# Performance work log

Hardware: AMD Instinct MI355X
Metric: run time of the kernel (lower is better)

Reference implementation:

```python
import jax, jax.numpy as jnp
import numpy as np

B, S, D, H = 2, 2048, 1024, 16
DH = D // H  # 64, matches Attention's hardcoded d_k=64 scale


def setup_inputs() -> dict:
    key = jax.random.key(0)
    kq, kk, kv, kw, kb = jax.random.split(key, 5)
    return {
        "q": jax.random.normal(kq, (B, S, D), dtype=jnp.float32),
        "k": jax.random.normal(kk, (B, S, D), dtype=jnp.float32),
        "v": jax.random.normal(kv, (B, S, D), dtype=jnp.float32),
        "w_o_w": jax.random.normal(kw, (D, D), dtype=jnp.float32) * 0.02,
        "w_o_b": jax.random.normal(kb, (D,), dtype=jnp.float32) * 0.02,
    }


def _to_heads(x):
    # [B,S,D] -> [B,H,S,DH]
    b, s, d = x.shape
    return x.reshape(b, s, H, DH).transpose(0, 2, 1, 3)


def reference(q, k, v, w_o_w, w_o_b):
    # pre-activation (F.relu) on raw q,k,v
    qh = _to_heads(jax.nn.relu(q))
    kh = _to_heads(jax.nn.relu(k))
    vh = _to_heads(jax.nn.relu(v))
    scale = 1.0 / jnp.sqrt(jnp.asarray(DH, dtype=q.dtype))
    # naive attention: full [B,H,S,S] score matrix, softmax over keys
    scores = jnp.einsum("bhsd,bhtd->bhst", qh, kh) * scale
    probs = jax.nn.softmax(scores, axis=-1)
    attn = jnp.einsum("bhst,bhtd->bhsd", probs, vh)
    # merge heads: [B,H,S,DH] -> [B,S,D]
    out = attn.transpose(0, 2, 1, 3).reshape(B, S, D)
    # output projection (nn.Linear applies x @ W.T + b) then post-activation
    out = out @ w_o_w.T + w_o_b
    return jax.nn.relu(out)
```

## Files before the change

kernel.cpp:

```cpp
#include <hip/hip_runtime.h>
#include <hip/hip_bf16.h>

#define Bc 2
#define Hc 16
#define Sc 2048
#define Dc 1024

typedef __attribute__((ext_vector_type(8))) short s16x8;
typedef __attribute__((ext_vector_type(4))) float f32x4;
typedef __attribute__((ext_vector_type(16))) float f32x16;

#define AS1 __attribute__((address_space(1)))
#define AS3 __attribute__((address_space(3)))

static __device__ __forceinline__ float fexp2(float x) {
#if __has_builtin(__builtin_amdgcn_exp2f)
    return __builtin_amdgcn_exp2f(x);
#else
    float r; asm("v_exp_f32 %0, %1" : "=v"(r) : "v"(x)); return r;
#endif
}

static __device__ __forceinline__ unsigned cvtpk(float lo, float hi) {
    unsigned r; asm("v_cvt_pk_bf16_f32 %0, %1, %2" : "=v"(r) : "v"(lo), "v"(hi));
    return r;
}

static __device__ __forceinline__ void plswap(unsigned &x, unsigned &y) {
#if __has_builtin(__builtin_amdgcn_permlane32_swap)
    typedef __attribute__((ext_vector_type(2))) unsigned int u32x2;
    u32x2 t = __builtin_amdgcn_permlane32_swap(x, y, false, false);
    x = t.x; y = t.y;
#else
    asm volatile("v_permlane32_swap_b32 %0, %1" : "+v"(x), "+v"(y));
#endif
}

static __device__ __forceinline__ unsigned short f2bf(float f) {
    union { float f; unsigned u; } x; x.f = f;
    unsigned r = x.u + 0x7fffu + ((x.u >> 16) & 1u);
    return (unsigned short)(r >> 16);
}

__global__ __launch_bounds__(256) void relu_cvt_heads(const float* __restrict__ src,
                                                      unsigned short* __restrict__ dst,
                                                      float scale) {
    long i = ((long)blockIdx.x * blockDim.x + threadIdx.x) * 4;
    if (i >= (long)Bc * Sc * Dc) return;
    int dh = (int)(i & 63);
    int h  = (int)((i >> 6) & (Hc - 1));
    int s  = (int)((i >> 10) & (Sc - 1));
    int b  = (int)(i >> 21);
    float4 v = *reinterpret_cast<const float4*>(src + i);
    long o = (((long)b * Hc + h) * Sc + s) * 64 + dh;
    ushort4 w;
    w.x = f2bf(fmaxf(v.x, 0.f) * scale);
    w.y = f2bf(fmaxf(v.y, 0.f) * scale);
    w.z = f2bf(fmaxf(v.z, 0.f) * scale);
    w.w = f2bf(fmaxf(v.w, 0.f) * scale);
    *reinterpret_cast<ushort4*>(dst + o) = w;
}

__global__ __launch_bounds__(256) void relu_cvt_vT(const float* __restrict__ v,
                                                   unsigned short* __restrict__ vt) {
    __shared__ unsigned short lds[64][66];
    const int tid = threadIdx.x;
    const int st = blockIdx.x & (Sc / 64 - 1);
    const int bh = blockIdx.x >> 5;
    const int b = bh >> 4, h = bh & 15;
#pragma unroll
    for (int i = 0; i < 4; ++i) {
        int srow = (tid >> 4) + i * 16;
        int scol = (tid & 15) * 4;
        float4 x = *(const float4*)(v + ((long)b * Sc + st * 64 + srow) * Dc + h * 64 + scol);
        lds[srow][scol + 0] = f2bf(fmaxf(x.x, 0.f));
        lds[srow][scol + 1] = f2bf(fmaxf(x.y, 0.f));
        lds[srow][scol + 2] = f2bf(fmaxf(x.z, 0.f));
        lds[srow][scol + 3] = f2bf(fmaxf(x.w, 0.f));
    }
    __syncthreads();
#pragma unroll
    for (int i = 0; i < 2; ++i) {
        int dh = (tid >> 3) + i * 32;
        int sc = (tid & 7) * 8;
        union { unsigned short u[8]; s16x8 v8; } o;
#pragma unroll
        for (int j = 0; j < 8; ++j) o.u[j] = lds[sc + j][dh];
        *(s16x8*)(vt + ((long)bh * 64 + dh) * Sc + st * 64 + sc) = o.v8;
    }
}

__global__ __launch_bounds__(256) void cvt_w(const float* __restrict__ src,
                                             unsigned short* __restrict__ dst) {
    long i = ((long)blockIdx.x * blockDim.x + threadIdx.x) * 4;
    if (i >= (long)Dc * Dc) return;
    float4 v = *reinterpret_cast<const float4*>(src + i);
    ushort4 w;
    w.x = f2bf(v.x); w.y = f2bf(v.y); w.z = f2bf(v.z); w.w = f2bf(v.w);
    *reinterpret_cast<ushort4*>(dst + i) = w;
}

__global__ __launch_bounds__(256, 2) void attn_lds(const unsigned short* __restrict__ qh,
                                                   const unsigned short* __restrict__ kh,
                                                   const unsigned short* __restrict__ vt,
                                                   unsigned short* __restrict__ xout) {
    __shared__ unsigned short Klds[2][64 * 64];
    __shared__ unsigned short Vlds[2][64 * 64];

    const int tid = threadIdx.x;
    const int l = tid & 63, w = tid >> 6;
    const int r32 = l & 31, hl = l >> 5;
    const int job = (blockIdx.x & 7) * 64 + (blockIdx.x >> 3);
    const int qb = job & 15;
    const int bh = job >> 4;

    const unsigned short* Qp = qh + ((long)bh * Sc + qb * 128 + w * 32) * 64;
    const unsigned short* Kp = kh + (long)bh * Sc * 64;
    const unsigned short* Vp = vt + (long)bh * 64 * Sc;

    s16x8 qbf[4];
#pragma unroll
    for (int ds = 0; ds < 4; ++ds)
        qbf[ds] = *(const s16x8*)(Qp + r32 * 64 + ds * 16 + hl * 8);

    f32x16 acc0 = {0,0,0,0,0,0,0,0,0,0,0,0,0,0,0,0};
    f32x16 acc1 = {0,0,0,0,0,0,0,0,0,0,0,0,0,0,0,0};
    float denom = 0.f;

    auto stage = [&](int buf, int kv0) {
#pragma unroll
        for (int j = 0; j < 2; ++j) {
            const int cbase = w * 64 + j * 256;
            const int chunk = cbase + l;
            const int row = chunk >> 3, cc = chunk & 7;
            const int scc = cc ^ (row & 7);
            const unsigned short* ksrc = Kp + (long)(kv0 + row) * 64 + scc * 8;
            const unsigned short* vsrc = Vp + (long)row * Sc + kv0 + scc * 8;
            __builtin_amdgcn_global_load_lds((const AS1 unsigned int*)(const void*)ksrc,
                                             (AS3 unsigned int*)(void*)&Klds[buf][cbase * 8],
                                             16, 0, 0);
            __builtin_amdgcn_global_load_lds((const AS1 unsigned int*)(const void*)vsrc,
                                             (AS3 unsigned int*)(void*)&Vlds[buf][cbase * 8],
                                             16, 0, 0);
        }
    };

    auto compute = [&](int buf) {
        const unsigned short* KB = &Klds[buf][0];
        const unsigned short* VB = &Vlds[buf][0];
        unsigned Bw[4][4];
#pragma unroll
        for (int kt = 0; kt < 2; ++kt) {
            f32x16 st = {0,0,0,0,0,0,0,0,0,0,0,0,0,0,0,0};
#pragma unroll
            for (int ds = 0; ds < 4; ++ds) {
                const int row = kt * 32 + r32;
                const int cc = ((ds * 2 + hl) ^ (row & 7));
                s16x8 ka = *(const s16x8*)(KB + row * 64 + cc * 8);
                st = __builtin_amdgcn_mfma_f32_32x32x16_bf16(ka, qbf[ds], st, 0, 0, 0);
            }
            float p[16];
#pragma unroll
            for (int i = 0; i < 16; ++i) p[i] = fexp2(st[i]);
            denom += (((p[0] + p[1]) + (p[2] + p[3])) + ((p[4] + p[5]) + (p[6] + p[7])))
                   + (((p[8] + p[9]) + (p[10] + p[11])) + ((p[12] + p[13]) + (p[14] + p[15])));
            unsigned a0 = cvtpk(p[0], p[1]),   b0 = cvtpk(p[2], p[3]);
            unsigned c0 = cvtpk(p[4], p[5]),   d0 = cvtpk(p[6], p[7]);
            unsigned a1 = cvtpk(p[8], p[9]),   b1 = cvtpk(p[10], p[11]);
            unsigned c1 = cvtpk(p[12], p[13]), d1 = cvtpk(p[14], p[15]);
            plswap(a0, c0); plswap(b0, d0);
            plswap(a1, c1); plswap(b1, d1);
            Bw[kt * 2 + 0][0] = a0; Bw[kt * 2 + 0][1] = b0;
            Bw[kt * 2 + 0][2] = c0; Bw[kt * 2 + 0][3] = d0;
            Bw[kt * 2 + 1][0] = a1; Bw[kt * 2 + 1][1] = b1;
            Bw[kt * 2 + 1][2] = c1; Bw[kt * 2 + 1][3] = d1;
        }
#pragma unroll
        for (int dt = 0; dt < 2; ++dt) {
#pragma unroll
            for (int s = 0; s < 4; ++s) {
                const int row = dt * 32 + r32;
                const int cc = ((s * 2 + hl) ^ (row & 7));
                s16x8 va = *(const s16x8*)(VB + row * 64 + cc * 8);
                union { unsigned u[4]; s16x8 v8; } bp;
                bp.u[0] = Bw[s][0]; bp.u[1] = Bw[s][1];
                bp.u[2] = Bw[s][2]; bp.u[3] = Bw[s][3];
                if (dt == 0)
                    acc0 = __builtin_amdgcn_mfma_f32_32x32x16_bf16(va, bp.v8, acc0, 0, 0, 0);
                else
                    acc1 = __builtin_amdgcn_mfma_f32_32x32x16_bf16(va, bp.v8, acc1, 0, 0, 0);
            }
        }
    };

    stage(0, 0);
    __syncthreads();
    int cur = 0;
    for (int t = 0; t < Sc / 64 - 1; ++t) {
        stage(cur ^ 1, (t + 1) * 64);
        compute(cur);
        __syncthreads();
        cur ^= 1;
    }
    compute(cur);

    float dn = denom + __shfl_xor(denom, 32);
    const float inv = 1.0f / dn;
    const int b = bh >> 4, h = bh & 15;
    unsigned short* Xrow = xout + ((long)b * Sc + qb * 128 + w * 32 + r32) * Dc + h * 64;
#pragma unroll
    for (int dt = 0; dt < 2; ++dt) {
        const f32x16& A = dt ? acc1 : acc0;
#pragma unroll
        for (int rg = 0; rg < 4; ++rg) {
            unsigned wlo = cvtpk(A[rg * 4 + 0] * inv, A[rg * 4 + 1] * inv);
            unsigned whi = cvtpk(A[rg * 4 + 2] * inv, A[rg * 4 + 3] * inv);
            uint2 wv; wv.x = wlo; wv.y = whi;
            *reinterpret_cast<uint2*>(Xrow + dt * 32 + rg * 8 + hl * 4) = wv;
        }
    }
}

__global__ __launch_bounds__(256, 2) void proj128(const unsigned short* __restrict__ X,
                                                  const unsigned short* __restrict__ Wb,
                                                  const float* __restrict__ bias,
                                                  float* __restrict__ out) {
    __shared__ unsigned short Xlds[2][128 * 64];
    __shared__ unsigned short Wlds[2][64 * 64];

    const int tid = threadIdx.x;
    const int l = tid & 63, w = tid >> 6;
    const int r32 = l & 31, hl = l >> 5;
    const int job = (blockIdx.x & 7) * 64 + (blockIdx.x >> 3);
    const int nb = job & 15;
    const int mb = job >> 4;

    const unsigned short* Xp = X + (long)mb * 128 * Dc;
    const unsigned short* Wp = Wb + (long)nb * 64 * Dc;

    f32x16 acc0 = {0,0,0,0,0,0,0,0,0,0,0,0,0,0,0,0};
    f32x16 acc1 = {0,0,0,0,0,0,0,0,0,0,0,0,0,0,0,0};

    auto stage = [&](int buf, int k0) {
#pragma unroll
        for (int j = 0; j < 4; ++j) {
            const int cbase = w * 256 + j * 64;
            const int chunk = cbase + l;
            const int row = chunk >> 3, cc = chunk & 7;
            const int scc = cc ^ (row & 7);
            const unsigned short* xsrc = Xp + (long)row * Dc + k0 + scc * 8;
            __builtin_amdgcn_global_load_lds((const AS1 unsigned int*)(const void*)xsrc,
                                             (AS3 unsigned int*)(void*)&Xlds[buf][cbase * 8],
                                             16, 0, 0);
        }
#pragma unroll
        for (int j = 0; j < 2; ++j) {
            const int cbase = w * 128 + j * 64;
            const int chunk = cbase + l;
            const int row = chunk >> 3, cc = chunk & 7;
            const int scc = cc ^ (row & 7);
            const unsigned short* wsrc = Wp + (long)row * Dc + k0 + scc * 8;
            __builtin_amdgcn_global_load_lds((const AS1 unsigned int*)(const void*)wsrc,
                                             (AS3 unsigned int*)(void*)&Wlds[buf][cbase * 8],
                                             16, 0, 0);
        }
    };

    auto compute = [&](int buf) {
        const unsigned short* XB = &Xlds[buf][0];
        const unsigned short* WB = &Wlds[buf][0];
#pragma unroll
        for (int ks = 0; ks < 4; ++ks) {
            const int arow = w * 32 + r32;
            const int acc_ = ((ks * 2 + hl) ^ (arow & 7));
            s16x8 af = *(const s16x8*)(XB + arow * 64 + acc_ * 8);
#pragma unroll
            for (int nt = 0; nt < 2; ++nt) {
                const int brow = nt * 32 + r32;
                const int bcc = ((ks * 2 + hl) ^ (brow & 7));
                s16x8 bf = *(const s16x8*)(WB + brow * 64 + bcc * 8);
                if (nt == 0)
                    acc0 = __builtin_amdgcn_mfma_f32_32x32x16_bf16(af, bf, acc0, 0, 0, 0);
                else
                    acc1 = __builtin_amdgcn_mfma_f32_32x32x16_bf16(af, bf, acc1, 0, 0, 0);
            }
        }
    };

    stage(0, 0);
    __syncthreads();
    int cur = 0;
    for (int t = 0; t < Dc / 64 - 1; ++t) {
        stage(cur ^ 1, (t + 1) * 64);
        compute(cur);
        __syncthreads();
        cur ^= 1;
    }
    compute(cur);

#pragma unroll
    for (int nt = 0; nt < 2; ++nt) {
        const f32x16& A = nt ? acc1 : acc0;
        const float bv = bias[nb * 64 + nt * 32 + r32];
#pragma unroll
        for (int j = 0; j < 16; ++j) {
            const int m = (j & 3) + 8 * (j >> 2) + 4 * hl;
            out[((long)(mb * 128 + w * 32 + m)) * Dc + nb * 64 + nt * 32 + r32] =
                fmaxf(A[j] + bv, 0.f);
        }
    }
}

extern "C" void kernel_launch(void* const* d_in, const int* in_sizes, int n_in,
                              void* d_out, int out_size, void* d_ws, size_t ws_size,
                              hipStream_t stream) {
    const float* q    = (const float*)d_in[0];
    const float* k    = (const float*)d_in[1];
    const float* v    = (const float*)d_in[2];
    const float* w    = (const float*)d_in[3];
    const float* bias = (const float*)d_in[4];
    float* out = (float*)d_out;

    unsigned short* ws = (unsigned short*)d_ws;
    unsigned short* qh = ws;
    unsigned short* kh = qh + 4194304;
    unsigned short* vt = kh + 4194304;
    unsigned short* wb = vt + 4194304;
    unsigned short* X  = wb + 1048576;

    const float QSCALE = 0.125f * 1.44269504088896340736f;
    relu_cvt_heads<<<4096, 256, 0, stream>>>(q, qh, QSCALE);
    relu_cvt_heads<<<4096, 256, 0, stream>>>(k, kh, 1.0f);
    relu_cvt_vT<<<1024, 256, 0, stream>>>(v, vt);
    cvt_w<<<1024, 256, 0, stream>>>(w, wb);
    attn_lds<<<Bc * Hc * (Sc / 128), 256, 0, stream>>>(qh, kh, vt, X);
    proj128<<<(Bc * Sc / 128) * (Dc / 64), 256, 0, stream>>>(X, wb, bias, out);
}
```

Measured before the change: 83.21 us.

## Fuse prep kernels, stagger attention KV start, widen projection tile to 128

The four preprocessing kernels (Q/K relu-convert-to-heads, V transpose, weight convert) are merged into one launch that dispatches on block index. This removes three kernel launches and their tail gaps. The attention kernel now starts each block's KV loop at a different tile offset, spreading concurrent blocks across different K/V memory. The output projection tile grows from 128x64 to 128x128 with four accumulators per wave, raising MFMA work per LDS load at the cost of more registers and LDS and fewer blocks.

New measurement: 81.89 us, median of 2. No clear change (-1.6%).

```diff
diff --git a/kernel.cpp b/kernel.cpp
--- a/kernel.cpp
+++ b/kernel.cpp
@@ -42,62 +42,68 @@
     return (unsigned short)(r >> 16);
 }
 
-__global__ __launch_bounds__(256) void relu_cvt_heads(const float* __restrict__ src,
-                                                      unsigned short* __restrict__ dst,
-                                                      float scale) {
-    long i = ((long)blockIdx.x * blockDim.x + threadIdx.x) * 4;
-    if (i >= (long)Bc * Sc * Dc) return;
-    int dh = (int)(i & 63);
-    int h  = (int)((i >> 6) & (Hc - 1));
-    int s  = (int)((i >> 10) & (Sc - 1));
-    int b  = (int)(i >> 21);
-    float4 v = *reinterpret_cast<const float4*>(src + i);
-    long o = (((long)b * Hc + h) * Sc + s) * 64 + dh;
-    ushort4 w;
-    w.x = f2bf(fmaxf(v.x, 0.f) * scale);
-    w.y = f2bf(fmaxf(v.y, 0.f) * scale);
-    w.z = f2bf(fmaxf(v.z, 0.f) * scale);
-    w.w = f2bf(fmaxf(v.w, 0.f) * scale);
-    *reinterpret_cast<ushort4*>(dst + o) = w;
-}
-
-__global__ __launch_bounds__(256) void relu_cvt_vT(const float* __restrict__ v,
-                                                   unsigned short* __restrict__ vt) {
-    __shared__ unsigned short lds[64][66];
+__global__ __launch_bounds__(256) void prep_all(const float* __restrict__ q,
+                                                const float* __restrict__ k,
+                                                const float* __restrict__ v,
+                                                const float* __restrict__ w,
+                                                unsigned short* __restrict__ qh,
+                                                unsigned short* __restrict__ kh,
+                                                unsigned short* __restrict__ vt,
+                                                unsigned short* __restrict__ wb) {
+    const int bid = blockIdx.x;
     const int tid = threadIdx.x;
-    const int st = blockIdx.x & (Sc / 64 - 1);
-    const int bh = blockIdx.x >> 5;
-    const int b = bh >> 4, h = bh & 15;
-#pragma unroll
-    for (int i = 0; i < 4; ++i) {
-        int srow = (tid >> 4) + i * 16;
-        int scol = (tid & 15) * 4;
-        float4 x = *(const float4*)(v + ((long)b * Sc + st * 64 + srow) * Dc + h * 64 + scol);
-        lds[srow][scol + 0] = f2bf(fmaxf(x.x, 0.f));
-        lds[srow][scol + 1] = f2bf(fmaxf(x.y, 0.f));
-        lds[srow][scol + 2] = f2bf(fmaxf(x.z, 0.f));
-        lds[srow][scol + 3] = f2bf(fmaxf(x.w, 0.f));
-    }
-    __syncthreads();
-#pragma unroll
-    for (int i = 0; i < 2; ++i) {
-        int dh = (tid >> 3) + i * 32;
-        int sc = (tid & 7) * 8;
-        union { unsigned short u[8]; s16x8 v8; } o;
-#pragma unroll
-        for (int j = 0; j < 8; ++j) o.u[j] = lds[sc + j][dh];
-        *(s16x8*)(vt + ((long)bh * 64 + dh) * Sc + st * 64 + sc) = o.v8;
-    }
-}
-
-__global__ __launch_bounds__(256) void cvt_w(const float* __restrict__ src,
-                                             unsigned short* __restrict__ dst) {
-    long i = ((long)blockIdx.x * blockDim.x + threadIdx.x) * 4;
-    if (i >= (long)Dc * Dc) return;
-    float4 v = *reinterpret_cast<const float4*>(src + i);
-    ushort4 w;
-    w.x = f2bf(v.x); w.y = f2bf(v.y); w.z = f2bf(v.z); w.w = f2bf(v.w);
-    *reinterpret_cast<ushort4*>(dst + i) = w;
+    if (bid < 8192) {
+        const bool isQ = bid < 4096;
+        const float* src = isQ ? q : k;
+        unsigned short* dst = isQ ? qh : kh;
+        const float scale = isQ ? 0.18033688011112042f : 1.0f;
+        long i = ((long)(bid & 4095) * 256 + tid) * 4;
+        int dh = (int)(i & 63);
+        int h  = (int)((i >> 6) & (Hc - 1));
+        int s  = (int)((i >> 10) & (Sc - 1));
+        int b  = (int)(i >> 21);
+        float4 x = *reinterpret_cast<const float4*>(src + i);
+        long o = (((long)b * Hc + h) * Sc + s) * 64 + dh;
+        ushort4 r;
+        r.x = f2bf(fmaxf(x.x, 0.f) * scale);
+        r.y = f2bf(fmaxf(x.y, 0.f) * scale);
+        r.z = f2bf(fmaxf(x.z, 0.f) * scale);
+        r.w = f2bf(fmaxf(x.w, 0.f) * scale);
+        *reinterpret_cast<ushort4*>(dst + o) = r;
+    } else if (bid < 9216) {
+        __shared__ unsigned short lds[64][66];
+        const int lb = bid - 8192;
+        const int st = lb & (Sc / 64 - 1);
+        const int bh = lb >> 5;
+        const int b = bh >> 4, h = bh & 15;
+#pragma unroll
+        for (int i = 0; i < 4; ++i) {
+            int srow = (tid >> 4) + i * 16;
+            int scol = (tid & 15) * 4;
+            float4 x = *(const float4*)(v + ((long)b * Sc + st * 64 + srow) * Dc + h * 64 + scol);
+            lds[srow][scol + 0] = f2bf(fmaxf(x.x, 0.f));
+            lds[srow][scol + 1] = f2bf(fmaxf(x.y, 0.f));
+            lds[srow][scol + 2] = f2bf(fmaxf(x.z, 0.f));
+            lds[srow][scol + 3] = f2bf(fmaxf(x.w, 0.f));
+        }
+        __syncthreads();
+#pragma unroll
+        for (int i = 0; i < 2; ++i) {
+            int dh = (tid >> 3) + i * 32;
+            int sc = (tid & 7) * 8;
+            union { unsigned short u[8]; s16x8 v8; } o;
+#pragma unroll
+            for (int j = 0; j < 8; ++j) o.u[j] = lds[sc + j][dh];
+            *(s16x8*)(vt + ((long)bh * 64 + dh) * Sc + st * 64 + sc) = o.v8;
+        }
+    } else {
+        const int lb = bid - 9216;
+        long i = ((long)lb * 256 + tid) * 4;
+        float4 x = *reinterpret_cast<const float4*>(w + i);
+        ushort4 r;
+        r.x = f2bf(x.x); r.y = f2bf(x.y); r.z = f2bf(x.z); r.w = f2bf(x.w);
+        *reinterpret_cast<ushort4*>(wb + i) = r;
+    }
 }
 
 __global__ __launch_bounds__(256, 2) void attn_lds(const unsigned short* __restrict__ qh,
@@ -113,6 +119,7 @@
     const int job = (blockIdx.x & 7) * 64 + (blockIdx.x >> 3);
     const int qb = job & 15;
     const int bh = job >> 4;
+    const int phase = job & 31;
 
     const unsigned short* Qp = qh + ((long)bh * Sc + qb * 128 + w * 32) * 64;
     const unsigned short* Kp = kh + (long)bh * Sc * 64;
@@ -193,11 +200,11 @@
         }
     };
 
-    stage(0, 0);
+    stage(0, phase * 64);
     __syncthreads();
     int cur = 0;
     for (int t = 0; t < Sc / 64 - 1; ++t) {
-        stage(cur ^ 1, (t + 1) * 64);
+        stage(cur ^ 1, ((t + 1 + phase) & (Sc / 64 - 1)) * 64);
         compute(cur);
         __syncthreads();
         cur ^= 1;
@@ -221,47 +228,41 @@
     }
 }
 
-__global__ __launch_bounds__(256, 2) void proj128(const unsigned short* __restrict__ X,
+__global__ __launch_bounds__(256, 2) void proj256(const unsigned short* __restrict__ X,
                                                   const unsigned short* __restrict__ Wb,
                                                   const float* __restrict__ bias,
                                                   float* __restrict__ out) {
     __shared__ unsigned short Xlds[2][128 * 64];
-    __shared__ unsigned short Wlds[2][64 * 64];
+    __shared__ unsigned short Wlds[2][128 * 64];
 
     const int tid = threadIdx.x;
     const int l = tid & 63, w = tid >> 6;
     const int r32 = l & 31, hl = l >> 5;
-    const int job = (blockIdx.x & 7) * 64 + (blockIdx.x >> 3);
-    const int nb = job & 15;
-    const int mb = job >> 4;
+    const int job = (blockIdx.x & 7) * 32 + (blockIdx.x >> 3);
+    const int nb = job & 7;
+    const int mb = job >> 3;
 
     const unsigned short* Xp = X + (long)mb * 128 * Dc;
-    const unsigned short* Wp = Wb + (long)nb * 64 * Dc;
-
-    f32x16 acc0 = {0,0,0,0,0,0,0,0,0,0,0,0,0,0,0,0};
-    f32x16 acc1 = {0,0,0,0,0,0,0,0,0,0,0,0,0,0,0,0};
+    const unsigned short* Wp = Wb + (long)nb * 128 * Dc;
+
+    f32x16 acc[4];
+#pragma unroll
+    for (int nt = 0; nt < 4; ++nt)
+        acc[nt] = (f32x16){0,0,0,0,0,0,0,0,0,0,0,0,0,0,0,0};
 
     auto stage = [&](int buf, int k0) {
 #pragma unroll
         for (int j = 0; j < 4; ++j) {
-            const int cbase = w * 256 + j * 64;
-            const int chunk = cbase + l;
+            const int chunk = j * 256 + tid;
             const int row = chunk >> 3, cc = chunk & 7;
             const int scc = cc ^ (row & 7);
             const unsigned short* xsrc = Xp + (long)row * Dc + k0 + scc * 8;
+            const unsigned short* wsrc = Wp + (long)row * Dc + k0 + scc * 8;
             __builtin_amdgcn_global_load_lds((const AS1 unsigned int*)(const void*)xsrc,
-                                             (AS3 unsigned int*)(void*)&Xlds[buf][cbase * 8],
+                                             (AS3 unsigned int*)(void*)&Xlds[buf][chunk * 8],
                                              16, 0, 0);
-        }
-#pragma unroll
-        for (int j = 0; j < 2; ++j) {
-            const int cbase = w * 128 + j * 64;
-            const int chunk = cbase + l;
-            const int row = chunk >> 3, cc = chunk & 7;
-            const int scc = cc ^ (row & 7);
-            const unsigned short* wsrc = Wp + (long)row * Dc + k0 + scc * 8;
             __builtin_amdgcn_global_load_lds((const AS1 unsigned int*)(const void*)wsrc,
-                                             (AS3 unsigned int*)(void*)&Wlds[buf][cbase * 8],
+                                             (AS3 unsigned int*)(void*)&Wlds[buf][chunk * 8],
                                              16, 0, 0);
         }
     };
@@ -275,14 +276,11 @@
             const int acc_ = ((ks * 2 + hl) ^ (arow & 7));
             s16x8 af = *(const s16x8*)(XB + arow * 64 + acc_ * 8);
 #pragma unroll
-            for (int nt = 0; nt < 2; ++nt) {
+            for (int nt = 0; nt < 4; ++nt) {
                 const int brow = nt * 32 + r32;
                 const int bcc = ((ks * 2 + hl) ^ (brow & 7));
                 s16x8 bf = *(const s16x8*)(WB + brow * 64 + bcc * 8);
-                if (nt == 0)
-                    acc0 = __builtin_amdgcn_mfma_f32_32x32x16_bf16(af, bf, acc0, 0, 0, 0);
-                else
-                    acc1 = __builtin_amdgcn_mfma_f32_32x32x16_bf16(af, bf, acc1, 0, 0, 0);
+                acc[nt] = __builtin_amdgcn_mfma_f32_32x32x16_bf16(af, bf, acc[nt], 0, 0, 0);
             }
         }
     };
@@ -299,14 +297,13 @@
     compute(cur);
 
 #pragma unroll
-    for (int nt = 0; nt < 2; ++nt) {
-        const f32x16& A = nt ? acc1 : acc0;
-        const float bv = bias[nb * 64 + nt * 32 + r32];
+    for (int nt = 0; nt < 4; ++nt) {
+        const float bv = bias[nb * 128 + nt * 32 + r32];
 #pragma unroll
         for (int j = 0; j < 16; ++j) {
             const int m = (j & 3) + 8 * (j >> 2) + 4 * hl;
-            out[((long)(mb * 128 + w * 32 + m)) * Dc + nb * 64 + nt * 32 + r32] =
-                fmaxf(A[j] + bv, 0.f);
+            out[((long)(mb * 128 + w * 32 + m)) * Dc + nb * 128 + nt * 32 + r32] =
+                fmaxf(acc[nt][j] + bv, 0.f);
         }
     }
 }
@@ -328,11 +325,7 @@
     unsigned short* wb = vt + 4194304;
     unsigned short* X  = wb + 1048576;
 
-    const float QSCALE = 0.125f * 1.44269504088896340736f;
-    relu_cvt_heads<<<4096, 256, 0, stream>>>(q, qh, QSCALE);
-    relu_cvt_heads<<<4096, 256, 0, stream>>>(k, kh, 1.0f);
-    relu_cvt_vT<<<1024, 256, 0, stream>>>(v, vt);
-    cvt_w<<<1024, 256, 0, stream>>>(w, wb);
+    prep_all<<<10240, 256, 0, stream>>>(q, k, v, w, qh, kh, vt, wb);
     attn_lds<<<Bc * Hc * (Sc / 128), 256, 0, stream>>>(qh, kh, vt, X);
-    proj128<<<(Bc * Sc / 128) * (Dc / 64), 256, 0, stream>>>(X, wb, bias, out);
-}
+    proj256<<<(Bc * Sc / 128) * (Dc / 128), 256, 0, stream>>>(X, wb, bias, out);
+}
```
